# Optimization experiments

Measured on AMD Instinct MI355X. Metric: run time of the kernel, lower is better.

## Reference

```python
import jax, jax.numpy as jnp
import numpy as np

# ---- dopri5 (RK45) tableau ----
C2, C3, C4, C5 = 1/5, 3/10, 4/5, 8/9
A21 = 1/5
A31, A32 = 3/40, 9/40
A41, A42, A43 = 44/45, -56/15, 32/9
A51, A52, A53, A54 = 19372/6561, -25360/2187, 64448/6561, -212/729
A61, A62, A63, A64, A65 = 9017/3168, -355/33, 46732/5247, 49/176, -5103/18656
B1, B3, B4, B5, B6 = 35/384, 500/1113, 125/192, -2187/6784, 11/84
# error coefficients = b(5th) - b(4th)
E1, E3, E4, E5, E6, E7 = 71/57600, -71/16695, 71/1920, -17253/339200, 22/525, -1/40

N_STEPS = 24          # fixed scan length for the adaptive loop (jit-friendly)
RTOL = ATOL = 1e-3    # tolerance from init_kwargs
DT0 = 0.1             # initial step size


def conv_time(t, x, w, b, padding):
    # append time as an extra channel, then NCHW conv
    t_img = jnp.full_like(x[:, :1], t)
    xt = jnp.concatenate([t_img, x], axis=1)
    y = jax.lax.conv_general_dilated(xt, w, (1, 1), padding,
                                     dimension_numbers=('NCHW', 'OIHW', 'NCHW'))
    return y + b[None, :, None, None]


def ode_func(t, x, w1, b1, w2, b2, w3, b3):
    h = jax.nn.relu(conv_time(t, x, w1, b1, [(0, 0), (0, 0)]))
    h = jax.nn.relu(conv_time(t, h, w2, b2, [(1, 1), (1, 1)]))
    return conv_time(t, h, w3, b3, [(0, 0), (0, 0)])


def dopri5_step(f, t, y, dt):
    k1 = f(t, y)
    k2 = f(t + dt * C2, y + dt * (A21 * k1))
    k3 = f(t + dt * C3, y + dt * (A31 * k1 + A32 * k2))
    k4 = f(t + dt * C4, y + dt * (A41 * k1 + A42 * k2 + A43 * k3))
    k5 = f(t + dt * C5, y + dt * (A51 * k1 + A52 * k2 + A53 * k3 + A54 * k4))
    k6 = f(t + dt, y + dt * (A61 * k1 + A62 * k2 + A63 * k3 + A64 * k4 + A65 * k5))
    y5 = y + dt * (B1 * k1 + B3 * k3 + B4 * k4 + B5 * k5 + B6 * k6)
    k7 = f(t + dt, y5)  # FSAL stage, used for error estimate
    err = dt * (E1 * k1 + E3 * k3 + E4 * k4 + E5 * k5 + E6 * k6 + E7 * k7)
    return y5, err


def integrate(f, y0):
    """Adaptive dopri5 from t=0 to t=1 with fixed-length masked scan."""
    def step(carry, _):
        t, y, dt = carry
        dt_c = jnp.minimum(dt, 1.0 - t)
        y_new, err = dopri5_step(f, t, y, dt_c)
        tol = ATOL + RTOL * jnp.maximum(jnp.abs(y), jnp.abs(y_new))
        err_norm = jnp.sqrt(jnp.mean((err / tol) ** 2))
        done = t >= 1.0 - 1e-7
        adv = (err_norm <= 1.0) & (~done)
        t_n = jnp.where(adv, t + dt_c, t)
        y_n = jnp.where(adv, y_new, y)
        safe = jnp.maximum(err_norm, 1e-10)
        factor = jnp.clip(0.9 * safe ** (-0.2), 0.2, 10.0)
        dt_n = jnp.where(done, dt, dt_c * factor)
        return (t_n, y_n, dt_n), None

    step = jax.checkpoint(step)
    (t, y, dt), _ = jax.lax.scan(step,
                                 (jnp.float32(0.0), y0, jnp.float32(DT0)),
                                 None, length=N_STEPS)
    return y


def setup_inputs() -> dict:
    key = jax.random.key(0)
    ks = jax.random.split(key, 9)
    B, Cin, H, W = 64, 3, 32, 32
    AUG, NF = 5, 64
    CH = Cin + AUG  # 8
    x = jax.random.normal(ks[0], (B, Cin, H, W), dtype=jnp.float32)
    def wgt(k, shape):
        fan_in = shape[1] * shape[2] * shape[3]
        return jax.random.normal(k, shape, dtype=jnp.float32) / np.sqrt(fan_in).astype(np.float32)
    w1 = wgt(ks[1], (NF, CH + 1, 1, 1)); b1 = jnp.zeros((NF,), jnp.float32)
    w2 = wgt(ks[2], (NF, NF + 1, 3, 3)); b2 = jnp.zeros((NF,), jnp.float32)
    w3 = wgt(ks[3], (CH, NF + 1, 1, 1)); b3 = jnp.zeros((CH,), jnp.float32)
    flat = CH * H * W  # 8192
    wl = jax.random.normal(ks[4], (10, flat), dtype=jnp.float32) / np.sqrt(flat).astype(np.float32)
    bl = jnp.zeros((10,), jnp.float32)
    return {"x": x, "w1": w1, "b1": b1, "w2": w2, "b2": b2,
            "w3": w3, "b3": b3, "wl": wl, "bl": bl}


def reference(x, w1, b1, w2, b2, w3, b3, wl, bl):
    B, C, H, W = x.shape
    AUG = w3.shape[0] - C  # augmented channels
    aug = jnp.zeros((B, AUG, H, W), dtype=x.dtype)
    y0 = jnp.concatenate([x, aug], axis=1)
    f = lambda t, y: ode_func(t, y, w1, b1, w2, b2, w3, b3)
    yT = integrate(f, y0)                    # state at t = 1
    out = yT.reshape(B, -1) @ wl.T + bl      # final linear head
    return out
```

## Files before the change

### kernel.cpp

```cpp
#include <hip/hip_runtime.h>
#include <math.h>

namespace {
constexpr int BN = 64;
constexpr int HW = 1024;
constexpr int NS = BN*8*HW;

constexpr float C2f = 0.2f, C3f = 0.3f, C4f = 0.8f, C5f = (float)(8.0/9.0);
constexpr float A21 = 0.2f;
constexpr float A31 = (float)(3.0/40.0),  A32 = (float)(9.0/40.0);
constexpr float A41 = (float)(44.0/45.0), A42 = (float)(-56.0/15.0), A43 = (float)(32.0/9.0);
constexpr float A51 = (float)(19372.0/6561.0), A52 = (float)(-25360.0/2187.0),
                A53 = (float)(64448.0/6561.0), A54 = (float)(-212.0/729.0);
constexpr float A61 = (float)(9017.0/3168.0), A62 = (float)(-355.0/33.0),
                A63 = (float)(46732.0/5247.0), A64 = (float)(49.0/176.0),
                A65 = (float)(-5103.0/18656.0);
constexpr float B1c = (float)(35.0/384.0), B3c = (float)(500.0/1113.0),
                B4c = (float)(125.0/192.0), B5c = (float)(-2187.0/6784.0),
                B6c = (float)(11.0/84.0);
constexpr float E1c = (float)(71.0/57600.0), E3c = (float)(-71.0/16695.0),
                E4c = (float)(71.0/1920.0), E5c = (float)(-17253.0/339200.0),
                E6c = (float)(22.0/525.0),  E7c = (float)(-1.0/40.0);
constexpr float RTOL = 1e-3f, ATOL = 1e-3f;

constexpr size_t OFF_PART = 0;
constexpr size_t OFF_FLAG = 1024;
constexpr size_t OFF_CNT  = 1536;
constexpr size_t OFF_TSUM = 1600;
constexpr size_t OFF_W2P  = 2176;
constexpr size_t OFF_Y    = 20608;
constexpr size_t OFF_Y5   = OFF_Y  + (size_t)NS;
constexpr size_t OFF_K    = OFF_Y5 + (size_t)NS;
constexpr size_t OFF_WPK  = OFF_K + (size_t)7*NS;
constexpr size_t OFF_FT   = OFF_WPK + 1152;
constexpr size_t OFF_FB   = OFF_FT + 512;

constexpr int ACT_STRIDE = 272;
constexpr int H2_STRIDE  = 144;
}

__constant__ float g_cf[6][5] = {
    {A21, 0, 0, 0, 0},
    {A31, A32, 0, 0, 0},
    {A41, A42, A43, 0, 0},
    {A51, A52, A53, A54, 0},
    {A61, A62, A63, A64, A65},
    {0, 0, 0, 0, 0}};
__constant__ float g_ct[6] = {C2f, C3f, C4f, C5f, 1.0f, 1.0f};

typedef _Float16 hfrag8 __attribute__((ext_vector_type(8)));
typedef float f32x16 __attribute__((ext_vector_type(16)));

union HU { hfrag8 h; unsigned u[4]; uint4 v; };

__device__ __forceinline__ float ld_sysf(const float* p) {
    return __hip_atomic_load(p, __ATOMIC_RELAXED, __HIP_MEMORY_SCOPE_SYSTEM);
}
__device__ __forceinline__ float2 ld_sysf2(const float* p) {
    union { unsigned long long u; float2 f; } c;
    c.u = __hip_atomic_load((const unsigned long long*)p, __ATOMIC_RELAXED,
                            __HIP_MEMORY_SCOPE_SYSTEM);
    return c.f;
}
__device__ __forceinline__ void st_sysf(float* p, float v) {
    __hip_atomic_store(p, v, __ATOMIC_RELAXED, __HIP_MEMORY_SCOPE_SYSTEM);
}
__device__ __forceinline__ void st_sysf2(float* p, float a, float b) {
    union { unsigned long long u; float2 f; } c;
    c.f = make_float2(a, b);
    __hip_atomic_store((unsigned long long*)p, c.u, __ATOMIC_RELAXED,
                       __HIP_MEMORY_SCOPE_SYSTEM);
}

__device__ __forceinline__ void ld8(const float* p, float* v, bool sys) {
    if (sys) {
        #pragma unroll
        for (int h = 0; h < 4; h++) {
            float2 t = ld_sysf2(p + 2*h);
            v[2*h] = t.x; v[2*h+1] = t.y;
        }
    } else {
        float4 a = *(const float4*)p;
        float4 b = *(const float4*)(p + 4);
        v[0]=a.x; v[1]=a.y; v[2]=a.z; v[3]=a.w;
        v[4]=b.x; v[5]=b.y; v[6]=b.z; v[7]=b.w;
    }
}
__device__ __forceinline__ void st8(float* p, const float* v, bool sys) {
    if (sys) {
        st_sysf2(p,     v[0], v[1]);
        st_sysf2(p + 2, v[2], v[3]);
        st_sysf2(p + 4, v[4], v[5]);
        st_sysf2(p + 6, v[6], v[7]);
    } else {
        *(float4*)p       = make_float4(v[0], v[1], v[2], v[3]);
        *(float4*)(p + 4) = make_float4(v[4], v[5], v[6], v[7]);
    }
}

__global__ __launch_bounds__(256)
void k_init(const float* __restrict__ x, float* __restrict__ y,
            int* __restrict__ flags, int* __restrict__ flagT,
            int* __restrict__ flagB, const float* __restrict__ bl,
            float* __restrict__ out)
{
    int idx = blockIdx.x*256 + threadIdx.x;
    int b = idx >> 13, px = (idx >> 3) & 1023, c = idx & 7;
    y[idx] = (c < 3) ? x[(size_t)(b*3 + c)*1024 + px] : 0.0f;
    if (idx < 512) { flags[idx] = 0; flagT[idx] = 0; flagB[idx] = 0; }
    if (idx < 640) out[idx] = bl[idx % 10];
}

__global__ __launch_bounds__(256)
void k_prepack(const float* __restrict__ w1, const float* __restrict__ w2,
               const float* __restrict__ w3, _Float16* __restrict__ w2p,
               float* __restrict__ tsum, float* __restrict__ wpk)
{
    int gid = blockIdx.x*256 + threadIdx.x;
    if (gid < 36864) {
        int j    = gid & 7;
        int lane = (gid >> 3) & 63;
        int nt   = (gid >> 9) & 1;
        int ks   = (gid >> 10) & 3;
        int tap  = gid >> 12;
        int oc = nt*32 + (lane & 31);
        int kpos = ks*16 + (lane >> 5)*8 + j;
        int oct = kpos >> 5, q2b = (kpos >> 4) & 1, rr = kpos & 15;
        int ic = oct*32 + (rr & 3) + (q2b << 2) + ((rr >> 2) << 3);
        w2p[gid] = (_Float16)w2[oc*585 + (1 + ic)*9 + tap];
    }
    if (gid < 576) {
        int oc = gid & 63, combo = gid >> 6;
        int rcase = combo / 3, ccase = combo % 3;
        float s = 0.0f;
        for (int kh = 0; kh < 3; kh++) {
            if ((rcase == 1 && kh == 0) || (rcase == 2 && kh == 2)) continue;
            for (int kw = 0; kw < 3; kw++) {
                if ((ccase == 1 && kw == 0) || (ccase == 2 && kw == 2)) continue;
                s += w2[oc*585 + kh*3 + kw];
            }
        }
        tsum[gid] = s;
    }
    if (gid < 512) wpk[gid] = w1[(gid & 63)*9 + 1 + (gid >> 6)];
    if (gid < 64)  wpk[512 + gid] = w1[gid*9];
    if (gid < 512) wpk[576 + gid] = w3[(gid & 7)*65 + 1 + (gid >> 3)];
    if (gid < 8)   wpk[1088 + gid] = w3[gid*65];
}

__global__ void __launch_bounds__(256, 2)
k_ode(const float* __restrict__ b1, const float* __restrict__ b2,
      const float* __restrict__ b3, const _Float16* __restrict__ w2p,
      const float* __restrict__ tsumg, const float* __restrict__ wpk,
      const float* __restrict__ wl, float* __restrict__ ybuf,
      float* __restrict__ y5buf, float* __restrict__ kb,
      float* __restrict__ part, int* __restrict__ flags,
      int* __restrict__ flagT, int* __restrict__ flagB,
      float* __restrict__ out)
{
    __shared__ __align__(16) unsigned char s_pool[192*ACT_STRIDE];
    __shared__ __align__(16) unsigned char s_h2[128*H2_STRIDE];
    __shared__ float s_tsum[576];
    __shared__ float s_b2v[64], s_b1v[64], s_w10v[64];
    __shared__ float s_w30v[8], s_b3v[8];
    __shared__ float s_red[40];

    const int tid = threadIdx.x;
    const int nblk = gridDim.x;
    const int lane = tid & 63;
    const int m32 = lane & 31, q2 = lane >> 5;
    const int rp = tid >> 7;
    const int np = (tid >> 6) & 1;
    const int wid = tid >> 6;
    const bool lz32 = (lane == 32);
    const bool lz31 = (lane == 31);

    if (tid < 64) {
        s_b2v[tid] = b2[tid];
        s_b1v[tid] = b1[tid];
        s_w10v[tid] = wpk[512 + tid];
    }
    if (tid < 8) { s_w30v[tid] = wpk[1088 + tid]; s_b3v[tid] = b3[tid]; }
    for (int i = tid; i < 576; i += 256) s_tsum[i] = tsumg[i];
    __syncthreads();

    hfrag8 w1lo[2], w1hi[2];
    #pragma unroll
    for (int oct = 0; oct < 2; oct++)
        #pragma unroll
        for (int j = 0; j < 8; j++) {
            _Float16 wv = (_Float16)wpk[j*64 + oct*32 + m32];
            w1lo[oct][j] = q2 ? (_Float16)0.0f : wv;
            w1hi[oct][j] = q2 ? wv : (_Float16)0.0f;
        }
    hfrag8 w3f[4];
    #pragma unroll
    for (int kst = 0; kst < 4; kst++)
        #pragma unroll
        for (int j = 0; j < 8; j++) {
            int kpos = kst*16 + q2*8 + j;
            int oct = kpos >> 5, q2b = (kpos >> 4) & 1, rr = kpos & 15;
            int ch = oct*32 + (rr & 3) + (q2b << 2) + ((rr >> 2) << 3);
            w3f[kst][j] = (m32 < 8) ? (_Float16)wpk[576 + ch*8 + m32]
                                    : (_Float16)0.0f;
        }

    float t = 0.0f, dt = 0.1f;
    float* ya = ybuf; float* yb = y5buf;
    float* ka = kb;  float* kg = kb + 6*(size_t)NS;

    auto wait_all = [&](int target) {
        for (;;) {
            bool ok = (__hip_atomic_load(&flags[tid], __ATOMIC_RELAXED,
                           __HIP_MEMORY_SCOPE_SYSTEM) >= target)
                   && (__hip_atomic_load(&flags[tid + 256], __ATOMIC_RELAXED,
                           __HIP_MEMORY_SCOPE_SYSTEM) >= target);
            if (__syncthreads_and((int)ok)) break;
            __builtin_amdgcn_s_sleep(2);
        }
    };

    auto eval = [&](const float* src, int nc, const float* cf, float ctv,
                    float* kout, int mode, int gev, float* partp) {
        float dtc = fminf(dt, 1.0f - t);
        float ts  = t + ctv*dtc;

        for (int tile = blockIdx.x; tile < 512; tile += nblk) {
            int b = tile >> 3, rg = tile & 7;

            auto zload = [&](int lr) {
                HU pz; pz.v = make_uint4(0u,0u,0u,0u);
                int r = rg*4 - 1 + lr;
                if ((unsigned)lr < 6u && (unsigned)r < 32u) {
                    bool nbr = (lr == 0) | (lr == 5);
                    int px = (r << 5) + m32;
                    size_t pb8 = ((size_t)(b << 10) + px) << 3;
                    float kv[5][8], sv[8];
                    if (nbr) {
                        #pragma unroll
                        for (int j = 0; j < 5; j++) if (j < nc) {
                            const float* kp = (j == 0 ? ka : kb + (size_t)j*NS) + pb8;
                            #pragma unroll
                            for (int h = 0; h < 4; h++) {
                                float2 t2 = ld_sysf2(kp + 2*h);
                                kv[j][2*h] = t2.x; kv[j][2*h+1] = t2.y;
                            }
                        }
                        #pragma unroll
                        for (int h = 0; h < 4; h++) {
                            float2 t2 = ld_sysf2(src + pb8 + 2*h);
                            sv[2*h] = t2.x; sv[2*h+1] = t2.y;
                        }
                    } else {
                        #pragma unroll
                        for (int j = 0; j < 5; j++) if (j < nc) {
                            const float* kp = (j == 0 ? ka : kb + (size_t)j*NS) + pb8;
                            float4 a4 = *(const float4*)kp;
                            float4 b4 = *(const float4*)(kp + 4);
                            kv[j][0]=a4.x; kv[j][1]=a4.y; kv[j][2]=a4.z; kv[j][3]=a4.w;
                            kv[j][4]=b4.x; kv[j][5]=b4.y; kv[j][6]=b4.z; kv[j][7]=b4.w;
                        }
                        float4 a4 = *(const float4*)(src + pb8);
                        float4 b4 = *(const float4*)(src + pb8 + 4);
                        sv[0]=a4.x; sv[1]=a4.y; sv[2]=a4.z; sv[3]=a4.w;
                        sv[4]=b4.x; sv[5]=b4.y; sv[6]=b4.z; sv[7]=b4.w;
                    }
                    float s_[8] = {0,0,0,0,0,0,0,0};
                    #pragma unroll
                    for (int j = 0; j < 5; j++) if (j < nc) {
                        float a = cf[j];
                        #pragma unroll
                        for (int c = 0; c < 8; c++) s_[c] = fmaf(a, kv[j][c], s_[c]);
                    }
                    #pragma unroll
                    for (int c = 0; c < 8; c++)
                        pz.h[c] = (_Float16)(sv[c] + dtc*s_[c]);
                }
                return pz;
            };

            HU pz;
            if (q2 == 0) pz = zload(wid + 1);
            if (gev > 1 && q2 == 1 && (wid == 0 || wid == 3)) {
                bool need = (wid == 0) ? (rg > 0) : (rg < 7);
                if (need) {
                    const int* fp = (wid == 0) ? &flagB[tile-1] : &flagT[tile+1];
                    while (__hip_atomic_load(fp, __ATOMIC_RELAXED,
                                             __HIP_MEMORY_SCOPE_SYSTEM) < gev-1)
                        __builtin_amdgcn_s_sleep(1);
                }
            }
            if (q2 == 1) pz = zload((wid == 0) ? 0 : ((wid == 3) ? 5 : -1));

            auto wr_act = [&](int lr, const f32x16& a1, int oct, bool valid) {
                unsigned words[8];
                #pragma unroll
                for (int pr = 0; pr < 8; pr++) {
                    int r0 = 2*pr;
                    int oc0 = oct*32 + (r0 & 3) + 8*(r0 >> 2) + 4*q2;
                    float v0 = valid ? fmaxf(a1[r0]   + ts*s_w10v[oc0]
                                             + s_b1v[oc0],   0.0f) : 0.0f;
                    float v1 = valid ? fmaxf(a1[r0+1] + ts*s_w10v[oc0+1]
                                             + s_b1v[oc0+1], 0.0f) : 0.0f;
                    union { _Float16 h[2]; unsigned u; } pk;
                    pk.h[0] = (_Float16)v0; pk.h[1] = (_Float16)v1;
                    words[pr] = pk.u;
                }
                unsigned char* basep = s_pool + (size_t)(lr*32 + m32)*ACT_STRIDE
                                       + oct*64 + q2*32;
                *(uint4*)basep        = make_uint4(words[0],words[1],words[2],words[3]);
                *(uint4*)(basep + 16) = make_uint4(words[4],words[5],words[6],words[7]);
            };
            {
                f32x16 zz = (f32x16)(0.0f);
                f32x16 c0 = __builtin_amdgcn_mfma_f32_32x32x16_f16(w1lo[0], pz.h, zz, 0,0,0);
                f32x16 c1 = __builtin_amdgcn_mfma_f32_32x32x16_f16(w1lo[1], pz.h, zz, 0,0,0);
                wr_act(wid + 1, c0, 0, true);
                wr_act(wid + 1, c1, 1, true);
                if (wid == 0 || wid == 3) {
                    int lrh = (wid == 0) ? 0 : 5;
                    bool vh = (unsigned)(rg*4 - 1 + lrh) < 32u;
                    f32x16 d0 = __builtin_amdgcn_mfma_f32_32x32x16_f16(w1hi[0], pz.h, zz, 0,0,0);
                    f32x16 d1 = __builtin_amdgcn_mfma_f32_32x32x16_f16(w1hi[1], pz.h, zz, 0,0,0);
                    wr_act(lrh, d0, 0, vh);
                    wr_act(lrh, d1, 1, vh);
                }
            }
            __syncthreads();

            f32x16 acc2[2];
            acc2[0] = (f32x16)(0.0f);
            acc2[1] = (f32x16)(0.0f);
            {
                const unsigned char* actb = (const unsigned char*)s_pool;
                #pragma unroll 1
                for (int ks = 0; ks < 4; ks++) {
                    HU fc[4], d0[4], d2[4];
                    #pragma unroll
                    for (int l = 0; l < 4; l++) {
                        const unsigned char* p = actb
                            + (size_t)((rp*2 + l)*32 + m32)*ACT_STRIDE
                            + ks*32 + q2*16;
                        fc[l].v = *(const uint4*)p;
                    }
                    #pragma unroll
                    for (int l = 0; l < 4; l++) {
                        #pragma unroll
                        for (int i = 0; i < 4; i++) {
                            unsigned s0 = (unsigned)__builtin_amdgcn_update_dpp(
                                0, (int)fc[l].u[i], 0x138, 0xF, 0xF, true);
                            d0[l].u[i] = lz32 ? 0u : s0;
                            unsigned s2 = (unsigned)__builtin_amdgcn_update_dpp(
                                0, (int)fc[l].u[i], 0x130, 0xF, 0xF, true);
                            d2[l].u[i] = lz31 ? 0u : s2;
                        }
                    }
                    #pragma unroll
                    for (int kh = 0; kh < 3; kh++) {
                        #pragma unroll
                        for (int kw = 0; kw < 3; kw++) {
                            int tap = kh*3 + kw;
                            hfrag8 aw = *(const hfrag8*)
                                (w2p + (size_t)((tap*4 + ks)*2 + np)*512 + lane*8);
                            #pragma unroll
                            for (int ri = 0; ri < 2; ri++) {
                                int l = ri + kh;
                                hfrag8 bf = (kw == 0) ? d0[l].h
                                          : ((kw == 1) ? fc[l].h : d2[l].h);
                                acc2[ri] = __builtin_amdgcn_mfma_f32_32x32x16_f16(
                                    aw, bf, acc2[ri], 0, 0, 0);
                            }
                        }
                    }
                }
            }

            {
                int ccase = (m32 == 0) ? 1 : ((m32 == 31) ? 2 : 0);
                #pragma unroll
                for (int ri = 0; ri < 2; ri++) {
                    int pg = rp*2 + ri;
                    int r_out = rg*4 + pg;
                    int rcase = (r_out == 0) ? 1 : ((r_out == 31) ? 2 : 0);
                    const float* tsb = &s_tsum[(rcase*3 + ccase)*64];
                    int px = pg*32 + m32;
                    unsigned words[8];
                    #pragma unroll
                    for (int pr = 0; pr < 8; pr++) {
                        int r0 = 2*pr;
                        int oc0 = np*32 + (r0 & 3) + 8*(r0 >> 2) + 4*q2;
                        float v0 = fmaxf(acc2[ri][r0]   + ts*tsb[oc0]
                                         + s_b2v[oc0],   0.0f);
                        float v1 = fmaxf(acc2[ri][r0+1] + ts*tsb[oc0+1]
                                         + s_b2v[oc0+1], 0.0f);
                        union { _Float16 h[2]; unsigned u; } pk;
                        pk.h[0] = (_Float16)v0; pk.h[1] = (_Float16)v1;
                        words[pr] = pk.u;
                    }
                    unsigned char* basep = s_h2 + (size_t)px*H2_STRIDE
                                           + np*64 + q2*32;
                    *(uint4*)basep        = make_uint4(words[0],words[1],words[2],words[3]);
                    *(uint4*)(basep + 16) = make_uint4(words[4],words[5],words[6],words[7]);
                }
            }
            __syncthreads();

            float ls = 0.0f;
            {
                f32x16 a3a = (f32x16)(0.0f);
                #pragma unroll
                for (int kst = 0; kst < 4; kst++) {
                    HU f;
                    const unsigned char* p = s_h2
                        + (size_t)(wid*32 + m32)*H2_STRIDE + kst*32 + q2*16;
                    f.v = *(const uint4*)p;
                    a3a = __builtin_amdgcn_mfma_f32_32x32x16_f16(
                        w3f[kst], f.h, a3a, 0, 0, 0);
                }
                float a3[8];
                #pragma unroll
                for (int r = 0; r < 4; r++) {
                    float own = a3a[r];
                    float oth = __shfl(own, lane ^ 32, 64);
                    a3[r]     = q2 ? oth : own;
                    a3[4 + r] = q2 ? own : oth;
                }
                if (q2 == 0) {
                    #pragma unroll
                    for (int c = 0; c < 8; c++)
                        a3[c] += fmaf(ts, s_w30v[c], s_b3v[c]);
                    bool edge = (wid == 0) | (wid == 3);
                    int px = rg*128 + wid*32 + m32;
                    size_t pb8 = ((size_t)(b << 10) + px) << 3;
                    st8(kout + pb8, a3, edge);
                    if (mode == 1) {
                        float kv1[8], kv3[8], kv4[8], kv5[8], yv[8], r8[8];
                        ld8(ka + pb8, kv1, false);
                        ld8(kb + 2*(size_t)NS + pb8, kv3, false);
                        ld8(kb + 3*(size_t)NS + pb8, kv4, false);
                        ld8(kb + 4*(size_t)NS + pb8, kv5, false);
                        ld8(ya + pb8, yv, false);
                        #pragma unroll
                        for (int c = 0; c < 8; c++)
                            r8[c] = yv[c] + dtc*(B1c*kv1[c] + B3c*kv3[c]
                                    + B4c*kv4[c] + B5c*kv5[c] + B6c*a3[c]);
                        st8(yb + pb8, r8, edge);
                    } else if (mode == 2) {
                        float kv1[8], kv3[8], kv4[8], kv5[8], kv6[8], yv[8], y5v[8];
                        ld8(ka + pb8, kv1, false);
                        ld8(kb + 2*(size_t)NS + pb8, kv3, false);
                        ld8(kb + 3*(size_t)NS + pb8, kv4, false);
                        ld8(kb + 4*(size_t)NS + pb8, kv5, false);
                        ld8(kb + 5*(size_t)NS + pb8, kv6, false);
                        ld8(ya + pb8, yv, false);
                        ld8(yb + pb8, y5v, false);
                        #pragma unroll
                        for (int c = 0; c < 8; c++) {
                            float e = dtc*(E1c*kv1[c] + E3c*kv3[c] + E4c*kv4[c]
                                           + E5c*kv5[c] + E6c*kv6[c] + E7c*a3[c]);
                            float tol = ATOL + RTOL*fmaxf(fabsf(yv[c]), fabsf(y5v[c]));
                            float rr = e / tol;
                            ls += rr*rr;
                        }
                    }
                }
            }
            asm volatile("s_waitcnt vmcnt(0)" ::: "memory");
            if (lane == 0 && wid == 0)
                __hip_atomic_store(&flagT[tile], gev, __ATOMIC_RELAXED,
                                   __HIP_MEMORY_SCOPE_SYSTEM);
            if (lane == 0 && wid == 3)
                __hip_atomic_store(&flagB[tile], gev, __ATOMIC_RELAXED,
                                   __HIP_MEMORY_SCOPE_SYSTEM);
            if (mode == 2) {
                float v = ls;
                #pragma unroll
                for (int off = 1; off < 64; off <<= 1)
                    v += __shfl_xor(v, off, 64);
                if (lane == 0) s_red[wid] = v;
                __syncthreads();
                if (tid == 0) {
                    st_sysf(&partp[tile],
                            s_red[0] + s_red[1] + s_red[2] + s_red[3]);
                    asm volatile("s_waitcnt vmcnt(0)" ::: "memory");
                    __hip_atomic_store(&flags[tile], gev, __ATOMIC_RELAXED,
                                       __HIP_MEMORY_SCOPE_SYSTEM);
                }
            }
        }
    };

    int gev = 1;
    eval(ya, 0, g_cf[5], 0.0f, ka, 0, gev, part);
    gev++;

    for (int st = 0; st < 24; st++) {
        if (t >= 1.0f - 1e-7f) break;
        float* partp = part + (size_t)(st & 1)*512;
        for (int e = 0; e < 6; e++) {
            int nc = (e < 5) ? e + 1 : 0;
            const float* src = (e == 5) ? yb : ya;
            float* kout = (e < 5) ? kb + (size_t)(e + 1)*NS : kg;
            int mode = (e == 4) ? 1 : ((e == 5) ? 2 : 0);
            eval(src, nc, g_cf[e], g_ct[e], kout, mode, gev, partp);
            gev++;
        }
        wait_all(gev - 1);
        float v = ld_sysf(&partp[tid]) + ld_sysf(&partp[tid + 256]);
        #pragma unroll
        for (int off = 1; off < 64; off <<= 1)
            v += __shfl_xor(v, off, 64);
        if (lane == 0) s_red[wid] = v;
        __syncthreads();
        float red0 = s_red[0] + s_red[1] + s_red[2] + s_red[3];
        float err_norm = sqrtf(red0 / (float)NS);
        float dtc = fminf(dt, 1.0f - t);
        bool adv = (err_norm <= 1.0f);
        if (adv) {
            t = t + dtc;
            float* tmp = ya; ya = yb; yb = tmp;
            tmp = ka; ka = kg; kg = tmp;
        }
        float safe = fmaxf(err_norm, 1e-10f);
        float factor = fminf(fmaxf(0.9f*powf(safe, -0.2f), 0.2f), 10.0f);
        dt = dtc*factor;
    }

    for (int tile = blockIdx.x; tile < 512; tile += nblk) {
        int b = tile >> 3, rg = tile & 7;
        if (tid < 128) {
            int lrow = tid >> 5;
            if (lrow == 1 || lrow == 2) {
                int px = rg*128 + tid;
                float* yp = ya + (((size_t)(b << 10) + px) << 3);
                float4 v0 = *(const float4*)yp;
                float4 v1 = *(const float4*)(yp + 4);
                st_sysf2(yp,     v0.x, v0.y);
                st_sysf2(yp + 2, v0.z, v0.w);
                st_sysf2(yp + 4, v1.x, v1.y);
                st_sysf2(yp + 6, v1.z, v1.w);
            }
        }
    }
    __syncthreads();
    for (int tile = blockIdx.x; tile < 512; tile += nblk)
        if (tid == 0)
            __hip_atomic_store(&flags[tile], gev, __ATOMIC_RELAXED,
                               __HIP_MEMORY_SCOPE_SYSTEM);
    wait_all(gev);

    for (int hb = blockIdx.x; hb < 256; hb += nblk) {
        int bh = hb >> 2, q = hb & 3;
        int px = q*256 + tid;
        const float* yp = ya + (((size_t)(bh << 10) + px) << 3);
        float acc[10];
        #pragma unroll
        for (int m = 0; m < 10; m++) acc[m] = 0.0f;
        float yv[8];
        #pragma unroll
        for (int h = 0; h < 4; h++) {
            float2 v = ld_sysf2(yp + 2*h);
            yv[2*h] = v.x; yv[2*h+1] = v.y;
        }
        #pragma unroll
        for (int c = 0; c < 8; c++) {
            float v = yv[c];
            #pragma unroll
            for (int m = 0; m < 10; m++)
                acc[m] = fmaf(v, wl[(size_t)m*8192 + (c << 10) + px], acc[m]);
        }
        #pragma unroll
        for (int m = 0; m < 10; m++) {
            float v = acc[m];
            #pragma unroll
            for (int off = 1; off < 64; off <<= 1)
                v += __shfl_xor(v, off, 64);
            acc[m] = v;
        }
        if (lane == 0) {
            #pragma unroll
            for (int m = 0; m < 10; m++) s_red[wid*10 + m] = acc[m];
        }
        __syncthreads();
        if (tid < 10) {
            float v = s_red[tid] + s_red[10 + tid]
                    + s_red[20 + tid] + s_red[30 + tid];
            atomicAdd(&out[bh*10 + tid], v);
        }
        __syncthreads();
    }
}

extern "C" void kernel_launch(void* const* d_in, const int* in_sizes, int n_in,
                              void* d_out, int out_size, void* d_ws, size_t ws_size,
                              hipStream_t stream)
{
    const float* x  = (const float*)d_in[0];
    const float* w1 = (const float*)d_in[1];
    const float* b1 = (const float*)d_in[2];
    const float* w2 = (const float*)d_in[3];
    const float* b2 = (const float*)d_in[4];
    const float* w3 = (const float*)d_in[5];
    const float* b3 = (const float*)d_in[6];
    const float* wl = (const float*)d_in[7];
    const float* bl = (const float*)d_in[8];
    float* out = (float*)d_out;

    float* F = (float*)d_ws;
    float* part = F + OFF_PART;
    int*   flags = (int*)(F + OFF_FLAG);
    float* tsum = F + OFF_TSUM;
    _Float16* w2p = (_Float16*)(F + OFF_W2P);
    float* y    = F + OFF_Y;
    float* y5   = F + OFF_Y5;
    float* kbp  = F + OFF_K;
    float* wpk  = F + OFF_WPK;
    int*   flagT = (int*)(F + OFF_FT);
    int*   flagB = (int*)(F + OFF_FB);

    k_init<<<NS/256, 256, 0, stream>>>(x, y, flags, flagT, flagB, bl, out);
    k_prepack<<<144, 256, 0, stream>>>(w1, w2, w3, w2p, tsum, wpk);

    int maxb = 0;
    if (hipOccupancyMaxActiveBlocksPerMultiprocessor(&maxb,
            reinterpret_cast<const void*>(k_ode), 256, 0) != hipSuccess || maxb < 1)
        maxb = 1;
    int cus = 256;
    {
        int dev = 0;
        hipGetDevice(&dev);
        hipDeviceProp_t prop;
        if (hipGetDeviceProperties(&prop, dev) == hipSuccess && prop.multiProcessorCount > 0)
            cus = prop.multiProcessorCount;
    }
    long cap = (long)maxb * (long)cus;
    int gridn = (int)((cap < 512) ? cap : 512);
    if (gridn < 16) gridn = 16;

    k_ode<<<gridn, 256, 0, stream>>>(b1, b2, b3, w2p, tsum, wpk, wl,
                                     y, y5, kbp, part, flags, flagT, flagB, out);
}
```

Baseline: 392.2 us.

## Pass halo rows between neighbor tiles via tagged mailboxes instead of flags

Edge warps now compute the next stage's input (y plus weighted k sum) for their boundary row and publish it to neighbor tiles as 64-bit tag|value words in a double-buffered mailbox. Consumers spin on the tags and read the halo directly, replacing the separate flag store, vmcnt wait and system-scope global halo loads. Edge k-stores use the cheaper non-system path except where they are still needed. This is meant to cut inter-block dependency latency in the persistent kernel, at the cost of extra loads and atomic stores on edge warps and more complex synchronisation.

```diff
diff --git a/kernel.cpp b/kernel.cpp
--- a/kernel.cpp
+++ b/kernel.cpp
@@ -34,6 +34,7 @@
 constexpr size_t OFF_WPK  = OFF_K + (size_t)7*NS;
 constexpr size_t OFF_FT   = OFF_WPK + 1152;
 constexpr size_t OFF_FB   = OFF_FT + 512;
+constexpr size_t OFF_MBX  = OFF_FB + 512;
 
 constexpr int ACT_STRIDE = 272;
 constexpr int H2_STRIDE  = 144;
@@ -102,13 +103,14 @@
 void k_init(const float* __restrict__ x, float* __restrict__ y,
             int* __restrict__ flags, int* __restrict__ flagT,
             int* __restrict__ flagB, const float* __restrict__ bl,
-            float* __restrict__ out)
+            float* __restrict__ out, unsigned long long* __restrict__ mbx)
 {
     int idx = blockIdx.x*256 + threadIdx.x;
     int b = idx >> 13, px = (idx >> 3) & 1023, c = idx & 7;
     y[idx] = (c < 3) ? x[(size_t)(b*3 + c)*1024 + px] : 0.0f;
     if (idx < 512) { flags[idx] = 0; flagT[idx] = 0; flagB[idx] = 0; }
     if (idx < 640) out[idx] = bl[idx % 10];
+    mbx[idx] = 0ull;
 }
 
 __global__ __launch_bounds__(256)
@@ -156,7 +158,7 @@
       float* __restrict__ y5buf, float* __restrict__ kb,
       float* __restrict__ part, int* __restrict__ flags,
       int* __restrict__ flagT, int* __restrict__ flagB,
-      float* __restrict__ out)
+      unsigned long long* __restrict__ mbx, float* __restrict__ out)
 {
     __shared__ __align__(16) unsigned char s_pool[192*ACT_STRIDE];
     __shared__ __align__(16) unsigned char s_h2[128*H2_STRIDE];
@@ -221,7 +223,7 @@
     };
 
     auto eval = [&](const float* src, int nc, const float* cf, float ctv,
-                    float* kout, int mode, int gev, float* partp) {
+                    float* kout, int mode, int gev, float* partp, int eidx) {
         float dtc = fminf(dt, 1.0f - t);
         float ts  = t + ctv*dtc;
 
@@ -281,16 +283,44 @@
 
             HU pz;
             if (q2 == 0) pz = zload(wid + 1);
-            if (gev > 1 && q2 == 1 && (wid == 0 || wid == 3)) {
-                bool need = (wid == 0) ? (rg > 0) : (rg < 7);
-                if (need) {
-                    const int* fp = (wid == 0) ? &flagB[tile-1] : &flagT[tile+1];
-                    while (__hip_atomic_load(fp, __ATOMIC_RELAXED,
-                                             __HIP_MEMORY_SCOPE_SYSTEM) < gev-1)
+            if (q2 == 1) {
+                bool nEx = (wid == 0) ? (rg > 0) : ((wid == 3) ? (rg < 7) : false);
+                if (eidx >= 1 && nEx) {
+                    int ntile = (wid == 0) ? tile - 1 : tile + 1;
+                    int nslot = (wid == 0) ? 1 : 0;
+                    const unsigned long long* mp = mbx +
+                        ((((size_t)(gev & 1)*512 + ntile)*2 + nslot)*32 + m32)*8;
+                    unsigned long long wv[8];
+                    for (;;) {
+                        bool ok = true;
+                        #pragma unroll
+                        for (int c = 0; c < 8; c++) {
+                            wv[c] = __hip_atomic_load(mp + c, __ATOMIC_RELAXED,
+                                                      __HIP_MEMORY_SCOPE_SYSTEM);
+                            ok = ok && ((int)((unsigned)(wv[c] >> 32)
+                                              - (unsigned)gev) >= 0);
+                        }
+                        if (ok) break;
                         __builtin_amdgcn_s_sleep(1);
-                }
-            }
-            if (q2 == 1) pz = zload((wid == 0) ? 0 : ((wid == 3) ? 5 : -1));
+                    }
+                    pz.v = make_uint4(0u,0u,0u,0u);
+                    #pragma unroll
+                    for (int c = 0; c < 8; c++) {
+                        union { unsigned u; float f; } cv;
+                        cv.u = (unsigned)wv[c];
+                        pz.h[c] = (_Float16)cv.f;
+                    }
+                } else {
+                    if (gev > 1 && eidx == 0 && nEx) {
+                        const int* fp = (wid == 0) ? &flagB[tile-1]
+                                                   : &flagT[tile+1];
+                        while (__hip_atomic_load(fp, __ATOMIC_RELAXED,
+                                                 __HIP_MEMORY_SCOPE_SYSTEM) < 1)
+                            __builtin_amdgcn_s_sleep(1);
+                    }
+                    pz = zload((wid == 0) ? 0 : ((wid == 3) ? 5 : -1));
+                }
+            }
 
             auto wr_act = [&](int lr, const f32x16& a1, int oct, bool valid) {
                 unsigned words[8];
@@ -432,9 +462,10 @@
                     bool edge = (wid == 0) | (wid == 3);
                     int px = rg*128 + wid*32 + m32;
                     size_t pb8 = ((size_t)(b << 10) + px) << 3;
-                    st8(kout + pb8, a3, edge);
+                    float r8[8];
+                    st8(kout + pb8, a3, edge && (mode == 2 || eidx == -1));
                     if (mode == 1) {
-                        float kv1[8], kv3[8], kv4[8], kv5[8], yv[8], r8[8];
+                        float kv1[8], kv3[8], kv4[8], kv5[8], yv[8];
                         ld8(ka + pb8, kv1, false);
                         ld8(kb + 2*(size_t)NS + pb8, kv3, false);
                         ld8(kb + 3*(size_t)NS + pb8, kv4, false);
@@ -463,16 +494,66 @@
                             ls += rr*rr;
                         }
                     }
-                }
-            }
-            asm volatile("s_waitcnt vmcnt(0)" ::: "memory");
-            if (lane == 0 && wid == 0)
-                __hip_atomic_store(&flagT[tile], gev, __ATOMIC_RELAXED,
-                                   __HIP_MEMORY_SCOPE_SYSTEM);
-            if (lane == 0 && wid == 3)
-                __hip_atomic_store(&flagB[tile], gev, __ATOMIC_RELAXED,
-                                   __HIP_MEMORY_SCOPE_SYSTEM);
+                    if (edge && eidx >= 0 && eidx <= 4) {
+                        bool nEx = (wid == 0) ? (rg > 0) : (rg < 7);
+                        if (nEx) {
+                            int enext = eidx + 1;
+                            float zn[8];
+                            if (enext == 5) {
+                                #pragma unroll
+                                for (int c = 0; c < 8; c++) zn[c] = r8[c];
+                            } else {
+                                float s2[8] = {0,0,0,0,0,0,0,0};
+                                #pragma unroll
+                                for (int j = 0; j < 4; j++) if (j < enext) {
+                                    const float* kp =
+                                        (j == 0 ? ka : kb + (size_t)j*NS) + pb8;
+                                    float kv[8];
+                                    ld8(kp, kv, false);
+                                    float a = g_cf[enext][j];
+                                    #pragma unroll
+                                    for (int c = 0; c < 8; c++)
+                                        s2[c] = fmaf(a, kv[c], s2[c]);
+                                }
+                                float alast = g_cf[enext][enext];
+                                #pragma unroll
+                                for (int c = 0; c < 8; c++)
+                                    s2[c] = fmaf(alast, a3[c], s2[c]);
+                                float sv[8];
+                                ld8(ya + pb8, sv, false);
+                                #pragma unroll
+                                for (int c = 0; c < 8; c++)
+                                    zn[c] = sv[c] + dtc*s2[c];
+                            }
+                            int eslot = (wid == 0) ? 0 : 1;
+                            unsigned long long* mp = mbx +
+                                ((((size_t)((gev + 1) & 1)*512 + tile)*2
+                                  + eslot)*32 + m32)*8;
+                            unsigned long long tg =
+                                ((unsigned long long)(unsigned)(gev + 1)) << 32;
+                            #pragma unroll
+                            for (int c = 0; c < 8; c++) {
+                                union { float f; unsigned u; } cv;
+                                cv.f = zn[c];
+                                __hip_atomic_store(mp + c, tg | cv.u,
+                                                   __ATOMIC_RELAXED,
+                                                   __HIP_MEMORY_SCOPE_SYSTEM);
+                            }
+                        }
+                    }
+                }
+            }
+            if (eidx == -1) {
+                asm volatile("s_waitcnt vmcnt(0)" ::: "memory");
+                if (lane == 0 && wid == 0)
+                    __hip_atomic_store(&flagT[tile], 1, __ATOMIC_RELAXED,
+                                       __HIP_MEMORY_SCOPE_SYSTEM);
+                if (lane == 0 && wid == 3)
+                    __hip_atomic_store(&flagB[tile], 1, __ATOMIC_RELAXED,
+                                       __HIP_MEMORY_SCOPE_SYSTEM);
+            }
             if (mode == 2) {
+                asm volatile("s_waitcnt vmcnt(0)" ::: "memory");
                 float v = ls;
                 #pragma unroll
                 for (int off = 1; off < 64; off <<= 1)
@@ -491,7 +572,7 @@
     };
 
     int gev = 1;
-    eval(ya, 0, g_cf[5], 0.0f, ka, 0, gev, part);
+    eval(ya, 0, g_cf[5], 0.0f, ka, 0, gev, part, -1);
     gev++;
 
     for (int st = 0; st < 24; st++) {
@@ -502,7 +583,7 @@
             const float* src = (e == 5) ? yb : ya;
             float* kout = (e < 5) ? kb + (size_t)(e + 1)*NS : kg;
             int mode = (e == 4) ? 1 : ((e == 5) ? 2 : 0);
-            eval(src, nc, g_cf[e], g_ct[e], kout, mode, gev, partp);
+            eval(src, nc, g_cf[e], g_ct[e], kout, mode, gev, partp, e);
             gev++;
         }
         wait_all(gev - 1);
@@ -617,8 +698,9 @@
     float* wpk  = F + OFF_WPK;
     int*   flagT = (int*)(F + OFF_FT);
     int*   flagB = (int*)(F + OFF_FB);
-
-    k_init<<<NS/256, 256, 0, stream>>>(x, y, flags, flagT, flagB, bl, out);
+    unsigned long long* mbx = (unsigned long long*)(F + OFF_MBX);
+
+    k_init<<<NS/256, 256, 0, stream>>>(x, y, flags, flagT, flagB, bl, out, mbx);
     k_prepack<<<144, 256, 0, stream>>>(w1, w2, w3, w2p, tsum, wpk);
 
     int maxb = 0;
@@ -638,5 +720,6 @@
     if (gridn < 16) gridn = 16;
 
     k_ode<<<gridn, 256, 0, stream>>>(b1, b2, b3, w2p, tsum, wpk, wl,
-                                     y, y5, kbp, part, flags, flagT, flagB, out);
-}
+                                     y, y5, kbp, part, flags, flagT, flagB,
+                                     mbx, out);
+}
```

After: 511.7 us. +30.5%, slower.
